# Kernel tuning notes

Measured on AMD Instinct MI355X. Metric: run time of the kernel, lower is better.

The kernel has to match this reference:

```python
import math
import jax, jax.numpy as jnp
from jax import lax
import numpy as np

L, B, S, H, N = 2, 1, 2048, 1024, 16
HN = H // N
EPS = 1e-5
SIGMA = 0.02
OUT_STD = SIGMA / math.sqrt(2.0 * L)


def gelu(x):
    # OpenAI tanh-approx gelu, matching gelu_impl
    return 0.5 * x * (1.0 + jnp.tanh(0.7978845608028654 * x * (1.0 + 0.044715 * x * x)))


def layer_norm(x, g, b):
    mu = jnp.mean(x, axis=-1, keepdims=True)
    var = jnp.mean(jnp.square(x - mu), axis=-1, keepdims=True)
    return (x - mu) / jnp.sqrt(var + EPS) * g + b


def setup_inputs() -> dict:
    key = jax.random.key(0)
    ks = jax.random.split(key, 8)
    x = jax.random.normal(ks[0], (B, S, H), dtype=jnp.float32)
    ltor_mask = jnp.tril(jnp.ones((S, S), dtype=jnp.float32))[None, None]  # [1,1,S,S]
    return {
        "hidden_states": x,
        "ltor_mask": ltor_mask,
        "ln1_g": jnp.ones((L, H), jnp.float32),
        "ln1_b": jnp.zeros((L, H), jnp.float32),
        "qkv_w": jax.random.normal(ks[1], (L, H, 3 * H), jnp.float32) * SIGMA,
        "qkv_b": jnp.zeros((L, 3 * H), jnp.float32),
        "dense_w": jax.random.normal(ks[2], (L, H, H), jnp.float32) * OUT_STD,
        "dense_b": jnp.zeros((L, H), jnp.float32),
        "ln2_g": jnp.ones((L, H), jnp.float32),
        "ln2_b": jnp.zeros((L, H), jnp.float32),
        "fc_w": jax.random.normal(ks[3], (L, H, 4 * H), jnp.float32) * SIGMA,
        "fc_b": jnp.zeros((L, 4 * H), jnp.float32),
        "proj_w": jax.random.normal(ks[4], (L, 4 * H, H), jnp.float32) * OUT_STD,
        "proj_b": jnp.zeros((L, H), jnp.float32),
        "lnf_g": jnp.ones((H,), jnp.float32),
        "lnf_b": jnp.zeros((H,), jnp.float32),
    }


def _transformer(hidden_states, ltor_mask, ln1_g, ln1_b, qkv_w, qkv_b, dense_w, dense_b,
                 ln2_g, ln2_b, fc_w, fc_b, proj_w, proj_b, lnf_g, lnf_b):
    scale = 1.0 / math.sqrt(HN)

    def step(h, p):
        g1, b1, qw, qb, dw, db, g2, b2, fw, fb, pw, pb = p
        y = layer_norm(h, g1, b1)
        qkv = y @ qw + qb                       # [B,S,3H]
        q, k, v = jnp.split(qkv, 3, axis=-1)
        # [B,S,H] -> [B,N,S,HN]
        q = q.reshape(B, S, N, HN).transpose(0, 2, 1, 3)
        k = k.reshape(B, S, N, HN).transpose(0, 2, 1, 3)
        v = v.reshape(B, S, N, HN).transpose(0, 2, 1, 3)
        scores = jnp.einsum('bnqd,bnkd->bnqk', q, k) * scale
        scores = scores * ltor_mask - 10000.0 * (1.0 - ltor_mask)
        probs = jax.nn.softmax(scores, axis=-1)
        ctx = jnp.einsum('bnqk,bnkd->bnqd', probs, v)
        ctx = ctx.transpose(0, 2, 1, 3).reshape(B, S, H)
        attn_out = ctx @ dw + db
        h2 = h + attn_out
        y2 = layer_norm(h2, g2, b2)
        mlp_out = gelu(y2 @ fw + fb) @ pw + pb
        return h2 + mlp_out, None

    params = (ln1_g, ln1_b, qkv_w, qkv_b, dense_w, dense_b,
              ln2_g, ln2_b, fc_w, fc_b, proj_w, proj_b)
    h, _ = lax.scan(step, hidden_states, params)
    return layer_norm(h, lnf_g, lnf_b)


def reference(hidden_states, ltor_mask, ln1_g, ln1_b, qkv_w, qkv_b, dense_w, dense_b,
              ln2_g, ln2_b, fc_w, fc_b, proj_w, proj_b, lnf_g, lnf_b):
    return _transformer(hidden_states, ltor_mask, ln1_g, ln1_b, qkv_w, qkv_b,
                        dense_w, dense_b, ln2_g, ln2_b, fc_w, fc_b,
                        proj_w, proj_b, lnf_g, lnf_b)
```

## Files before the change

kernel.cpp:

```cpp
#include <hip/hip_runtime.h>
#include <hip/hip_bf16.h>
#include <cstdint>
#include <cstddef>

typedef __bf16 bf16;
typedef __attribute__((ext_vector_type(4))) __bf16 bf16x4;
typedef __attribute__((ext_vector_type(8))) __bf16 bf16x8;
typedef __attribute__((ext_vector_type(4))) float floatx4;

__global__ __launch_bounds__(256) void ln_first(const float* __restrict__ x,
                                                float* __restrict__ h,
                                                const float* __restrict__ g,
                                                const float* __restrict__ b,
                                                bf16* __restrict__ y) {
    __shared__ float red[8];
    const int row = blockIdx.x, tid = threadIdx.x;
    const size_t off = (size_t)row * 1024 + tid * 4;
    const float4 v = *(const float4*)(x + off);
    *(float4*)(h + off) = v;
    float s = v.x + v.y + v.z + v.w;
#pragma unroll
    for (int o = 32; o > 0; o >>= 1) s += __shfl_xor(s, o);
    if ((tid & 63) == 0) red[tid >> 6] = s;
    __syncthreads();
    const float mean = (red[0] + red[1] + red[2] + red[3]) * (1.f / 1024.f);
    const float d[4] = {v.x - mean, v.y - mean, v.z - mean, v.w - mean};
    float q = d[0] * d[0] + d[1] * d[1] + d[2] * d[2] + d[3] * d[3];
#pragma unroll
    for (int o = 32; o > 0; o >>= 1) q += __shfl_xor(q, o);
    if ((tid & 63) == 0) red[4 + (tid >> 6)] = q;
    __syncthreads();
    const float var = (red[4] + red[5] + red[6] + red[7]) * (1.f / 1024.f);
    const float rstd = rsqrtf(var + 1e-5f);
    const int base = tid * 4;
#pragma unroll
    for (int i = 0; i < 4; i++)
        y[off + i] = (bf16)(d[i] * rstd * g[base + i] + b[base + i]);
}

template <typename OutT, int KS>
__global__ __launch_bounds__(256) void reduce_ln(const bf16* __restrict__ part,
                                                 const float* __restrict__ bias,
                                                 float* __restrict__ h,
                                                 const float* __restrict__ g,
                                                 const float* __restrict__ b,
                                                 OutT* __restrict__ y) {
    __shared__ float red[8];
    const int row = blockIdx.x, tid = threadIdx.x;
    const int base = tid * 4;
    const size_t off = (size_t)row * 1024 + base;
    const float4 hv = *(const float4*)(h + off);
    const float4 bv = *(const float4*)(bias + base);
    float a[4] = {hv.x + bv.x, hv.y + bv.y, hv.z + bv.z, hv.w + bv.w};
#pragma unroll
    for (int z = 0; z < KS; z++) {
        bf16x4 pv = *(const bf16x4*)(part + (size_t)z * (2048 * 1024) + off);
#pragma unroll
        for (int i = 0; i < 4; i++) a[i] += (float)pv[i];
    }
    *(float4*)(h + off) = (float4){a[0], a[1], a[2], a[3]};
    float s = a[0] + a[1] + a[2] + a[3];
#pragma unroll
    for (int o = 32; o > 0; o >>= 1) s += __shfl_xor(s, o);
    if ((tid & 63) == 0) red[tid >> 6] = s;
    __syncthreads();
    const float mean = (red[0] + red[1] + red[2] + red[3]) * (1.f / 1024.f);
    const float d[4] = {a[0] - mean, a[1] - mean, a[2] - mean, a[3] - mean};
    float q = d[0] * d[0] + d[1] * d[1] + d[2] * d[2] + d[3] * d[3];
#pragma unroll
    for (int o = 32; o > 0; o >>= 1) q += __shfl_xor(q, o);
    if ((tid & 63) == 0) red[4 + (tid >> 6)] = q;
    __syncthreads();
    const float var = (red[4] + red[5] + red[6] + red[7]) * (1.f / 1024.f);
    const float rstd = rsqrtf(var + 1e-5f);
#pragma unroll
    for (int i = 0; i < 4; i++)
        y[off + i] = (OutT)(d[i] * rstd * g[base + i] + b[base + i]);
}

__global__ __launch_bounds__(256) void transpose_cvt(const float* __restrict__ in,
                                                     bf16* __restrict__ out, int K, int N) {
    __shared__ float T[64][65];
    const int k0 = blockIdx.x * 64, n0 = blockIdx.y * 64;
    {
        const int r = threadIdx.x >> 4;
        const int c4 = (threadIdx.x & 15) * 4;
#pragma unroll
        for (int j = 0; j < 4; j++) {
            float4 v = *(const float4*)&in[(size_t)(k0 + r + j * 16) * N + n0 + c4];
            T[r + j * 16][c4 + 0] = v.x; T[r + j * 16][c4 + 1] = v.y;
            T[r + j * 16][c4 + 2] = v.z; T[r + j * 16][c4 + 3] = v.w;
        }
    }
    __syncthreads();
    {
        const int rn = threadIdx.x >> 3;
        const int c8 = (threadIdx.x & 7) * 8;
#pragma unroll
        for (int j = 0; j < 2; j++) {
            bf16x8 v;
#pragma unroll
            for (int i = 0; i < 8; i++) v[i] = (bf16)T[c8 + i][rn + j * 32];
            *(bf16x8*)&out[(size_t)(n0 + rn + j * 32) * K + k0 + c8] = v;
        }
    }
}

template <int MODE, int BM>
__global__ __launch_bounds__(256) void gemm_bt(const bf16* __restrict__ A,
                                               const bf16* __restrict__ BT,
                                               const float* __restrict__ bias,
                                               bf16* __restrict__ outb,
                                               int M, int N, int K) {
    constexpr int MS = BM / 32;
    constexpr int AC = BM / 32;
    constexpr int LS = 72;
    __shared__ bf16 As[BM * LS];
    __shared__ bf16 Bs[128 * LS];
    const int tid = threadIdx.x;
    const int w = tid >> 6, lane = tid & 63;
    const int quad = lane >> 4, l16 = lane & 15;
    const int wm = w >> 1, wn = w & 1;
    const int m0 = blockIdx.x * BM, n0 = blockIdx.y * 128;
    const int kchunk = K / gridDim.z;
    const int kbeg = blockIdx.z * kchunk, kend = kbeg + kchunk;

    const int srow = lane >> 3;
    const int scol = (lane & 7) * 8;
    const int arow = w * (BM / 4) + srow;
    const int brow = w * 32 + srow;
    const bf16* ga = A + (size_t)(m0 + arow) * K + scol;
    const bf16* gb = BT + (size_t)(n0 + brow) * K + scol;
    bf16* wa = &As[arow * LS + scol];
    bf16* wb = &Bs[brow * LS + scol];

    bf16x8 areg[AC], breg[4];
#pragma unroll
    for (int s = 0; s < AC; s++) areg[s] = *(const bf16x8*)(ga + (size_t)(s * 8) * K + kbeg);
#pragma unroll
    for (int s = 0; s < 4; s++) breg[s] = *(const bf16x8*)(gb + (size_t)(s * 8) * K + kbeg);

    floatx4 acc[MS][4];
#pragma unroll
    for (int i = 0; i < MS; i++)
#pragma unroll
        for (int j = 0; j < 4; j++) acc[i][j] = (floatx4){0.f, 0.f, 0.f, 0.f};

    for (int k0 = kbeg; k0 < kend; k0 += 64) {
        __syncthreads();
#pragma unroll
        for (int s = 0; s < AC; s++) *(bf16x8*)(wa + s * 8 * LS) = areg[s];
#pragma unroll
        for (int s = 0; s < 4; s++) *(bf16x8*)(wb + s * 8 * LS) = breg[s];
        __syncthreads();
        if (k0 + 64 < kend) {
#pragma unroll
            for (int s = 0; s < AC; s++) areg[s] = *(const bf16x8*)(ga + (size_t)(s * 8) * K + k0 + 64);
#pragma unroll
            for (int s = 0; s < 4; s++) breg[s] = *(const bf16x8*)(gb + (size_t)(s * 8) * K + k0 + 64);
        }
#pragma unroll
        for (int ks = 0; ks < 2; ks++) {
            bf16x8 af[MS], bfr[4];
#pragma unroll
            for (int ms = 0; ms < MS; ms++)
                af[ms] = *(const bf16x8*)&As[(wm * (BM / 2) + ms * 16 + l16) * LS + ks * 32 + quad * 8];
#pragma unroll
            for (int ns = 0; ns < 4; ns++)
                bfr[ns] = *(const bf16x8*)&Bs[(wn * 64 + ns * 16 + l16) * LS + ks * 32 + quad * 8];
#pragma unroll
            for (int ms = 0; ms < MS; ms++)
#pragma unroll
                for (int ns = 0; ns < 4; ns++)
                    acc[ms][ns] = __builtin_amdgcn_mfma_f32_16x16x32_bf16(af[ms], bfr[ns],
                                                                          acc[ms][ns], 0, 0, 0);
        }
    }

    bf16* pout = (MODE == 2) ? (outb + (size_t)blockIdx.z * M * N) : outb;
#pragma unroll
    for (int ms = 0; ms < MS; ms++) {
#pragma unroll
        for (int ns = 0; ns < 4; ns++) {
            const int row = m0 + wm * (BM / 2) + ms * 16 + quad * 4;
            const int col = n0 + wn * 64 + ns * 16 + l16;
            const float bv = (MODE == 2) ? 0.f : bias[col];
#pragma unroll
            for (int i = 0; i < 4; i++) {
                float v = acc[ms][ns][i] + bv;
                size_t idx = (size_t)(row + i) * N + col;
                if (MODE == 1) {
                    float t = 0.7978845608028654f * v * (1.f + 0.044715f * v * v);
                    pout[idx] = (bf16)(0.5f * v * (1.f + tanhf(t)));
                } else {
                    pout[idx] = (bf16)v;
                }
            }
        }
    }
}

__global__ __launch_bounds__(256) void attn_mfma(const bf16* __restrict__ qkv,
                                                 bf16* __restrict__ ctx) {
    __shared__ bf16 Ks[64][68];
    __shared__ bf16 Vt[64][72];
    __shared__ bf16 QPs[64][68];
    const int tid = threadIdx.x;
    const int w = tid >> 6, lane = tid & 63;
    const int quad = lane >> 4, l16 = lane & 15;
    const int head = blockIdx.y;
    const int qt = 31 - (int)blockIdx.x;
    const int qbase = qt * 64;
    const int rowg = w * 16 + quad * 4;

    const int r = tid >> 2;
    const int c = (tid & 3) * 16;

    {
        const bf16* qp = qkv + (size_t)(qbase + r) * 3072 + head * 64 + c;
        bf16x8 q0 = *(const bf16x8*)qp, q1 = *(const bf16x8*)(qp + 8);
        bf16x8 s0, s1;
#pragma unroll
        for (int i = 0; i < 8; i++) {
            s0[i] = (bf16)((float)q0[i] * 0.125f);
            s1[i] = (bf16)((float)q1[i] * 0.125f);
        }
        *(bf16x8*)&QPs[r][c] = s0;
        *(bf16x8*)&QPs[r][c + 8] = s1;
    }
    const bf16x8 aq0 = *(const bf16x8*)&QPs[w * 16 + l16][quad * 8];
    const bf16x8 aq1 = *(const bf16x8*)&QPs[w * 16 + l16][32 + quad * 8];

    float lsum[4] = {0.f, 0.f, 0.f, 0.f};
    floatx4 o[4];
#pragma unroll
    for (int d = 0; d < 4; d++) o[d] = (floatx4){0.f, 0.f, 0.f, 0.f};

    const int nt = qt + 1;
    bf16x8 kr0, kr1, vr0, vr1;
    {
        const bf16* kp = qkv + (size_t)r * 3072 + 1024 + head * 64 + c;
        kr0 = *(const bf16x8*)kp; kr1 = *(const bf16x8*)(kp + 8);
        const bf16* vp = qkv + (size_t)lane * 3072 + 2048 + head * 64 + w * 16;
        vr0 = *(const bf16x8*)vp; vr1 = *(const bf16x8*)(vp + 8);
    }

    for (int t = 0; t < nt; t++) {
        __syncthreads();
        *(bf16x8*)&Ks[r][c] = kr0;
        *(bf16x8*)&Ks[r][c + 8] = kr1;
#pragma unroll
        for (int i = 0; i < 8; i++) {
            Vt[w * 16 + i][lane] = vr0[i];
            Vt[w * 16 + 8 + i][lane] = vr1[i];
        }
        __syncthreads();
        if (t + 1 < nt) {
            const size_t kb = (size_t)(t + 1) * 64;
            const bf16* kp = qkv + (kb + r) * 3072 + 1024 + head * 64 + c;
            kr0 = *(const bf16x8*)kp; kr1 = *(const bf16x8*)(kp + 8);
            const bf16* vp = qkv + (kb + lane) * 3072 + 2048 + head * 64 + w * 16;
            vr0 = *(const bf16x8*)vp; vr1 = *(const bf16x8*)(vp + 8);
        }

        floatx4 s4[4];
#pragma unroll
        for (int n = 0; n < 4; n++) s4[n] = (floatx4){0.f, 0.f, 0.f, 0.f};
#pragma unroll
        for (int n = 0; n < 4; n++) {
            bf16x8 bk0 = *(const bf16x8*)&Ks[n * 16 + l16][quad * 8];
            bf16x8 bk1 = *(const bf16x8*)&Ks[n * 16 + l16][32 + quad * 8];
            s4[n] = __builtin_amdgcn_mfma_f32_16x16x32_bf16(aq0, bk0, s4[n], 0, 0, 0);
            s4[n] = __builtin_amdgcn_mfma_f32_16x16x32_bf16(aq1, bk1, s4[n], 0, 0, 0);
        }

        float p[4][4];
        if (t == qt) {
#pragma unroll
            for (int i = 0; i < 4; i++)
#pragma unroll
                for (int n = 0; n < 4; n++)
                    p[n][i] = (n * 16 + l16 > rowg + i) ? 0.f : __expf(s4[n][i]);
        } else {
#pragma unroll
            for (int i = 0; i < 4; i++)
#pragma unroll
                for (int n = 0; n < 4; n++)
                    p[n][i] = __expf(s4[n][i]);
        }
#pragma unroll
        for (int i = 0; i < 4; i++)
#pragma unroll
            for (int n = 0; n < 4; n++) lsum[i] += p[n][i];

#pragma unroll
        for (int n = 0; n < 4; n++)
#pragma unroll
            for (int i = 0; i < 4; i++)
                QPs[rowg + i][n * 16 + l16] = (bf16)p[n][i];

        bf16x8 ap0 = *(const bf16x8*)&QPs[w * 16 + l16][quad * 8];
        bf16x8 ap1 = *(const bf16x8*)&QPs[w * 16 + l16][32 + quad * 8];
#pragma unroll
        for (int d = 0; d < 4; d++) {
            bf16x8 bv0 = *(const bf16x8*)&Vt[d * 16 + l16][quad * 8];
            bf16x8 bv1 = *(const bf16x8*)&Vt[d * 16 + l16][32 + quad * 8];
            o[d] = __builtin_amdgcn_mfma_f32_16x16x32_bf16(ap0, bv0, o[d], 0, 0, 0);
            o[d] = __builtin_amdgcn_mfma_f32_16x16x32_bf16(ap1, bv1, o[d], 0, 0, 0);
        }
    }

#pragma unroll
    for (int i = 0; i < 4; i++)
#pragma unroll
        for (int msk = 1; msk < 16; msk <<= 1) lsum[i] += __shfl_xor(lsum[i], msk);

#pragma unroll
    for (int i = 0; i < 4; i++) {
        const float rl = 1.f / lsum[i];
        const size_t rb = (size_t)(qbase + rowg + i) * 1024 + head * 64;
#pragma unroll
        for (int d = 0; d < 4; d++)
            ctx[rb + d * 16 + l16] = (bf16)(o[d][i] * rl);
    }
}

extern "C" void kernel_launch(void* const* d_in, const int* in_sizes, int n_in,
                              void* d_out, int out_size, void* d_ws, size_t ws_size,
                              hipStream_t stream) {
    const float* hidden  = (const float*)d_in[0];
    const float* ln1_g   = (const float*)d_in[2];
    const float* ln1_b   = (const float*)d_in[3];
    const float* qkv_w   = (const float*)d_in[4];
    const float* qkv_b   = (const float*)d_in[5];
    const float* dense_w = (const float*)d_in[6];
    const float* dense_b = (const float*)d_in[7];
    const float* ln2_g   = (const float*)d_in[8];
    const float* ln2_b   = (const float*)d_in[9];
    const float* fc_w    = (const float*)d_in[10];
    const float* fc_b    = (const float*)d_in[11];
    const float* proj_w  = (const float*)d_in[12];
    const float* proj_b  = (const float*)d_in[13];
    const float* lnf_g   = (const float*)d_in[14];
    const float* lnf_b   = (const float*)d_in[15];

    char* ws = (char*)d_ws;
    float* h   = (float*)(ws);
    bf16* y    = (bf16*)(ws + 8u  * 1024 * 1024);
    bf16* qkv  = (bf16*)(ws + 12u * 1024 * 1024);
    bf16* ctx  = (bf16*)(ws + 24u * 1024 * 1024);
    bf16* mlp  = (bf16*)(ws + 12u * 1024 * 1024);
    bf16* wT   = (bf16*)(ws + 28u * 1024 * 1024);
    bf16* part = (bf16*)(ws + 36u * 1024 * 1024);

    ln_first<<<2048, 256, 0, stream>>>(hidden, h, ln1_g, ln1_b, y);

    for (int l = 0; l < 2; l++) {
        transpose_cvt<<<dim3(16, 48), 256, 0, stream>>>(qkv_w + (size_t)l * 1024 * 3072, wT, 1024, 3072);
        gemm_bt<0, 64><<<dim3(32, 24, 1), 256, 0, stream>>>(y, wT, qkv_b + l * 3072, qkv, 2048, 3072, 1024);

        attn_mfma<<<dim3(32, 16), 256, 0, stream>>>(qkv, ctx);

        transpose_cvt<<<dim3(16, 16), 256, 0, stream>>>(dense_w + (size_t)l * 1024 * 1024, wT, 1024, 1024);
        gemm_bt<2, 64><<<dim3(32, 8, 4), 256, 0, stream>>>(ctx, wT, nullptr, part, 2048, 1024, 1024);
        reduce_ln<bf16, 4><<<2048, 256, 0, stream>>>(part, dense_b + l * 1024, h,
                                                     ln2_g + l * 1024, ln2_b + l * 1024, y);

        transpose_cvt<<<dim3(16, 64), 256, 0, stream>>>(fc_w + (size_t)l * 1024 * 4096, wT, 1024, 4096);
        gemm_bt<1, 64><<<dim3(32, 32, 1), 256, 0, stream>>>(y, wT, fc_b + l * 4096, mlp, 2048, 4096, 1024);

        transpose_cvt<<<dim3(64, 16), 256, 0, stream>>>(proj_w + (size_t)l * 4096 * 1024, wT, 4096, 1024);
        gemm_bt<2, 64><<<dim3(32, 8, 4), 256, 0, stream>>>(mlp, wT, nullptr, part, 2048, 1024, 4096);
        if (l == 0) {
            reduce_ln<bf16, 4><<<2048, 256, 0, stream>>>(part, proj_b, h,
                                                         ln1_g + 1024, ln1_b + 1024, y);
        } else {
            reduce_ln<float, 4><<<2048, 256, 0, stream>>>(part, proj_b + 1024, h,
                                                          lnf_g, lnf_b, (float*)d_out);
        }
    }
}
```

Before: 508.2 us.

## Pair causal query tiles per block to balance attention work and share K/V

Each attention block now handles two query tiles, qt and 31-qt, so every block does the same total number of key tiles. The K/V tiles loaded into shared memory are reused by both query tiles, and the grid shrinks from 32x16 to 16x16 blocks. Softmax now uses exp2 with log2(e) folded into the Q scale, which is a cheaper instruction. In exchange the kernel uses more registers and shared memory, and the smaller grid of 256 blocks may underfill the GPU's compute units.

```diff
diff --git a/kernel.cpp b/kernel.cpp
--- a/kernel.cpp
+++ b/kernel.cpp
@@ -204,39 +204,48 @@
                                                  bf16* __restrict__ ctx) {
     __shared__ bf16 Ks[64][68];
     __shared__ bf16 Vt[64][72];
-    __shared__ bf16 QPs[64][68];
+    __shared__ bf16 QPa[64][68];
+    __shared__ bf16 QPb[64][68];
     const int tid = threadIdx.x;
     const int w = tid >> 6, lane = tid & 63;
     const int quad = lane >> 4, l16 = lane & 15;
     const int head = blockIdx.y;
-    const int qt = 31 - (int)blockIdx.x;
-    const int qbase = qt * 64;
+    const int qta = blockIdx.x;
+    const int qtb = 31 - qta;
+    const int qa = qta * 64, qb = qtb * 64;
     const int rowg = w * 16 + quad * 4;
-
     const int r = tid >> 2;
     const int c = (tid & 3) * 16;
+    const float SC = 0.18033688011111827f;
 
     {
-        const bf16* qp = qkv + (size_t)(qbase + r) * 3072 + head * 64 + c;
-        bf16x8 q0 = *(const bf16x8*)qp, q1 = *(const bf16x8*)(qp + 8);
-        bf16x8 s0, s1;
+        const bf16* pa = qkv + (size_t)(qa + r) * 3072 + head * 64 + c;
+        const bf16* pb = qkv + (size_t)(qb + r) * 3072 + head * 64 + c;
+        bf16x8 a0 = *(const bf16x8*)pa, a1 = *(const bf16x8*)(pa + 8);
+        bf16x8 b0 = *(const bf16x8*)pb, b1 = *(const bf16x8*)(pb + 8);
+        bf16x8 sa0, sa1, sb0, sb1;
 #pragma unroll
         for (int i = 0; i < 8; i++) {
-            s0[i] = (bf16)((float)q0[i] * 0.125f);
-            s1[i] = (bf16)((float)q1[i] * 0.125f);
-        }
-        *(bf16x8*)&QPs[r][c] = s0;
-        *(bf16x8*)&QPs[r][c + 8] = s1;
-    }
-    const bf16x8 aq0 = *(const bf16x8*)&QPs[w * 16 + l16][quad * 8];
-    const bf16x8 aq1 = *(const bf16x8*)&QPs[w * 16 + l16][32 + quad * 8];
-
-    float lsum[4] = {0.f, 0.f, 0.f, 0.f};
-    floatx4 o[4];
-#pragma unroll
-    for (int d = 0; d < 4; d++) o[d] = (floatx4){0.f, 0.f, 0.f, 0.f};
-
-    const int nt = qt + 1;
+            sa0[i] = (bf16)((float)a0[i] * SC); sa1[i] = (bf16)((float)a1[i] * SC);
+            sb0[i] = (bf16)((float)b0[i] * SC); sb1[i] = (bf16)((float)b1[i] * SC);
+        }
+        *(bf16x8*)&QPa[r][c] = sa0; *(bf16x8*)&QPa[r][c + 8] = sa1;
+        *(bf16x8*)&QPb[r][c] = sb0; *(bf16x8*)&QPb[r][c + 8] = sb1;
+    }
+    const bf16x8 aqA0 = *(const bf16x8*)&QPa[w * 16 + l16][quad * 8];
+    const bf16x8 aqA1 = *(const bf16x8*)&QPa[w * 16 + l16][32 + quad * 8];
+    const bf16x8 aqB0 = *(const bf16x8*)&QPb[w * 16 + l16][quad * 8];
+    const bf16x8 aqB1 = *(const bf16x8*)&QPb[w * 16 + l16][32 + quad * 8];
+
+    float lsa[4] = {0.f, 0.f, 0.f, 0.f}, lsb[4] = {0.f, 0.f, 0.f, 0.f};
+    floatx4 oa[4], ob[4];
+#pragma unroll
+    for (int d = 0; d < 4; d++) {
+        oa[d] = (floatx4){0.f, 0.f, 0.f, 0.f};
+        ob[d] = (floatx4){0.f, 0.f, 0.f, 0.f};
+    }
+
+    const int nt = qtb + 1;
     bf16x8 kr0, kr1, vr0, vr1;
     {
         const bf16* kp = qkv + (size_t)r * 3072 + 1024 + head * 64 + c;
@@ -262,66 +271,126 @@
             const bf16* vp = qkv + (kb + lane) * 3072 + 2048 + head * 64 + w * 16;
             vr0 = *(const bf16x8*)vp; vr1 = *(const bf16x8*)(vp + 8);
         }
-
-        floatx4 s4[4];
-#pragma unroll
-        for (int n = 0; n < 4; n++) s4[n] = (floatx4){0.f, 0.f, 0.f, 0.f};
+        const bool doA = (t <= qta);
+
+        floatx4 s4b[4], s4a[4];
+#pragma unroll
+        for (int n = 0; n < 4; n++) s4b[n] = (floatx4){0.f, 0.f, 0.f, 0.f};
 #pragma unroll
         for (int n = 0; n < 4; n++) {
             bf16x8 bk0 = *(const bf16x8*)&Ks[n * 16 + l16][quad * 8];
             bf16x8 bk1 = *(const bf16x8*)&Ks[n * 16 + l16][32 + quad * 8];
-            s4[n] = __builtin_amdgcn_mfma_f32_16x16x32_bf16(aq0, bk0, s4[n], 0, 0, 0);
-            s4[n] = __builtin_amdgcn_mfma_f32_16x16x32_bf16(aq1, bk1, s4[n], 0, 0, 0);
-        }
-
-        float p[4][4];
-        if (t == qt) {
+            s4b[n] = __builtin_amdgcn_mfma_f32_16x16x32_bf16(aqB0, bk0, s4b[n], 0, 0, 0);
+            s4b[n] = __builtin_amdgcn_mfma_f32_16x16x32_bf16(aqB1, bk1, s4b[n], 0, 0, 0);
+        }
+        if (doA) {
+#pragma unroll
+            for (int n = 0; n < 4; n++) s4a[n] = (floatx4){0.f, 0.f, 0.f, 0.f};
+#pragma unroll
+            for (int n = 0; n < 4; n++) {
+                bf16x8 bk0 = *(const bf16x8*)&Ks[n * 16 + l16][quad * 8];
+                bf16x8 bk1 = *(const bf16x8*)&Ks[n * 16 + l16][32 + quad * 8];
+                s4a[n] = __builtin_amdgcn_mfma_f32_16x16x32_bf16(aqA0, bk0, s4a[n], 0, 0, 0);
+                s4a[n] = __builtin_amdgcn_mfma_f32_16x16x32_bf16(aqA1, bk1, s4a[n], 0, 0, 0);
+            }
+        }
+
+        {
+            float p[4][4];
+            if (t == nt - 1) {
+#pragma unroll
+                for (int i = 0; i < 4; i++)
+#pragma unroll
+                    for (int n = 0; n < 4; n++)
+                        p[n][i] = (n * 16 + l16 > rowg + i) ? 0.f
+                                  : __builtin_amdgcn_exp2f(s4b[n][i]);
+            } else {
+#pragma unroll
+                for (int i = 0; i < 4; i++)
+#pragma unroll
+                    for (int n = 0; n < 4; n++)
+                        p[n][i] = __builtin_amdgcn_exp2f(s4b[n][i]);
+            }
 #pragma unroll
             for (int i = 0; i < 4; i++)
 #pragma unroll
-                for (int n = 0; n < 4; n++)
-                    p[n][i] = (n * 16 + l16 > rowg + i) ? 0.f : __expf(s4[n][i]);
-        } else {
+                for (int n = 0; n < 4; n++) lsb[i] += p[n][i];
+#pragma unroll
+            for (int n = 0; n < 4; n++)
+#pragma unroll
+                for (int i = 0; i < 4; i++)
+                    QPb[rowg + i][n * 16 + l16] = (bf16)p[n][i];
+        }
+        if (doA) {
+            float p[4][4];
+            if (t == qta) {
+#pragma unroll
+                for (int i = 0; i < 4; i++)
+#pragma unroll
+                    for (int n = 0; n < 4; n++)
+                        p[n][i] = (n * 16 + l16 > rowg + i) ? 0.f
+                                  : __builtin_amdgcn_exp2f(s4a[n][i]);
+            } else {
+#pragma unroll
+                for (int i = 0; i < 4; i++)
+#pragma unroll
+                    for (int n = 0; n < 4; n++)
+                        p[n][i] = __builtin_amdgcn_exp2f(s4a[n][i]);
+            }
 #pragma unroll
             for (int i = 0; i < 4; i++)
 #pragma unroll
-                for (int n = 0; n < 4; n++)
-                    p[n][i] = __expf(s4[n][i]);
-        }
-#pragma unroll
-        for (int i = 0; i < 4; i++)
-#pragma unroll
-            for (int n = 0; n < 4; n++) lsum[i] += p[n][i];
-
-#pragma unroll
-        for (int n = 0; n < 4; n++)
-#pragma unroll
-            for (int i = 0; i < 4; i++)
-                QPs[rowg + i][n * 16 + l16] = (bf16)p[n][i];
-
-        bf16x8 ap0 = *(const bf16x8*)&QPs[w * 16 + l16][quad * 8];
-        bf16x8 ap1 = *(const bf16x8*)&QPs[w * 16 + l16][32 + quad * 8];
+                for (int n = 0; n < 4; n++) lsa[i] += p[n][i];
+#pragma unroll
+            for (int n = 0; n < 4; n++)
+#pragma unroll
+                for (int i = 0; i < 4; i++)
+                    QPa[rowg + i][n * 16 + l16] = (bf16)p[n][i];
+        }
+
+        {
+            bf16x8 ap0 = *(const bf16x8*)&QPb[w * 16 + l16][quad * 8];
+            bf16x8 ap1 = *(const bf16x8*)&QPb[w * 16 + l16][32 + quad * 8];
+#pragma unroll
+            for (int d = 0; d < 4; d++) {
+                bf16x8 bv0 = *(const bf16x8*)&Vt[d * 16 + l16][quad * 8];
+                bf16x8 bv1 = *(const bf16x8*)&Vt[d * 16 + l16][32 + quad * 8];
+                ob[d] = __builtin_amdgcn_mfma_f32_16x16x32_bf16(ap0, bv0, ob[d], 0, 0, 0);
+                ob[d] = __builtin_amdgcn_mfma_f32_16x16x32_bf16(ap1, bv1, ob[d], 0, 0, 0);
+            }
+        }
+        if (doA) {
+            bf16x8 ap0 = *(const bf16x8*)&QPa[w * 16 + l16][quad * 8];
+            bf16x8 ap1 = *(const bf16x8*)&QPa[w * 16 + l16][32 + quad * 8];
+#pragma unroll
+            for (int d = 0; d < 4; d++) {
+                bf16x8 bv0 = *(const bf16x8*)&Vt[d * 16 + l16][quad * 8];
+                bf16x8 bv1 = *(const bf16x8*)&Vt[d * 16 + l16][32 + quad * 8];
+                oa[d] = __builtin_amdgcn_mfma_f32_16x16x32_bf16(ap0, bv0, oa[d], 0, 0, 0);
+                oa[d] = __builtin_amdgcn_mfma_f32_16x16x32_bf16(ap1, bv1, oa[d], 0, 0, 0);
+            }
+        }
+    }
+
+#pragma unroll
+    for (int i = 0; i < 4; i++) {
+#pragma unroll
+        for (int msk = 1; msk < 16; msk <<= 1) {
+            lsb[i] += __shfl_xor(lsb[i], msk);
+            lsa[i] += __shfl_xor(lsa[i], msk);
+        }
+    }
+#pragma unroll
+    for (int i = 0; i < 4; i++) {
+        const float rlb = 1.f / lsb[i];
+        const float rla = 1.f / lsa[i];
+        const size_t rbB = (size_t)(qb + rowg + i) * 1024 + head * 64;
+        const size_t rbA = (size_t)(qa + rowg + i) * 1024 + head * 64;
 #pragma unroll
         for (int d = 0; d < 4; d++) {
-            bf16x8 bv0 = *(const bf16x8*)&Vt[d * 16 + l16][quad * 8];
-            bf16x8 bv1 = *(const bf16x8*)&Vt[d * 16 + l16][32 + quad * 8];
-            o[d] = __builtin_amdgcn_mfma_f32_16x16x32_bf16(ap0, bv0, o[d], 0, 0, 0);
-            o[d] = __builtin_amdgcn_mfma_f32_16x16x32_bf16(ap1, bv1, o[d], 0, 0, 0);
-        }
-    }
-
-#pragma unroll
-    for (int i = 0; i < 4; i++)
-#pragma unroll
-        for (int msk = 1; msk < 16; msk <<= 1) lsum[i] += __shfl_xor(lsum[i], msk);
-
-#pragma unroll
-    for (int i = 0; i < 4; i++) {
-        const float rl = 1.f / lsum[i];
-        const size_t rb = (size_t)(qbase + rowg + i) * 1024 + head * 64;
-#pragma unroll
-        for (int d = 0; d < 4; d++)
-            ctx[rb + d * 16 + l16] = (bf16)(o[d][i] * rl);
+            ctx[rbB + d * 16 + l16] = (bf16)(ob[d][i] * rlb);
+            ctx[rbA + d * 16 + l16] = (bf16)(oa[d][i] * rla);
+        }
     }
 }
 
@@ -359,7 +428,7 @@
         transpose_cvt<<<dim3(16, 48), 256, 0, stream>>>(qkv_w + (size_t)l * 1024 * 3072, wT, 1024, 3072);
         gemm_bt<0, 64><<<dim3(32, 24, 1), 256, 0, stream>>>(y, wT, qkv_b + l * 3072, qkv, 2048, 3072, 1024);
 
-        attn_mfma<<<dim3(32, 16), 256, 0, stream>>>(qkv, ctx);
+        attn_mfma<<<dim3(16, 16), 256, 0, stream>>>(qkv, ctx);
 
         transpose_cvt<<<dim3(16, 16), 256, 0, stream>>>(dense_w + (size_t)l * 1024 * 1024, wT, 1024, 1024);
         gemm_bt<2, 64><<<dim3(32, 8, 4), 256, 0, stream>>>(ctx, wT, nullptr, part, 2048, 1024, 1024);
```

New measurement: 474.4 us. 1.07x faster.
